# Kernel optimization log

Hardware: AMD Instinct MI355X
Metric: run time of the kernel (lower is better)

## Reference

```python
import jax, jax.numpy as jnp
import numpy as np

H = 16          # num_heads
TOP_K = 2
LN_EPS = 1e-5


def setup_inputs() -> dict:
    key = jax.random.key(0)
    ks = jax.random.split(key, 8)
    B, S, E, NE = 2, 1024, 1024, 8
    w = lambda k, shp: jax.random.normal(k, shp, dtype=jnp.float32) * 0.02
    return {
        "x": jax.random.normal(ks[0], (B, S, E), dtype=jnp.float32),
        "rW1": w(ks[1], (E // 2, E)),
        "rb1": jnp.zeros((E // 2,), jnp.float32),
        "ln_g": jnp.ones((E // 2,), jnp.float32),
        "ln_b": jnp.zeros((E // 2,), jnp.float32),
        "rW2": w(ks[2], (NE, E // 2)),
        "rb2": jnp.zeros((NE,), jnp.float32),
        "qW": w(ks[3], (NE, E, E)),
        "qb": jnp.zeros((NE, E), jnp.float32),
        "kW": w(ks[4], (NE, E, E)),
        "kb": jnp.zeros((NE, E), jnp.float32),
        "vW": w(ks[5], (NE, E, E)),
        "vb": jnp.zeros((NE, E), jnp.float32),
        "oW": w(ks[6], (NE, E, E)),
        "ob": jnp.zeros((NE, E), jnp.float32),
    }


def reference(x, rW1, rb1, ln_g, ln_b, rW2, rb2, qW, qb, kW, kb, vW, vb, oW, ob):
    B, S, E = x.shape
    NE = qW.shape[0]
    Dh = E // H
    scale = 1.0 / jnp.sqrt(jnp.asarray(Dh, x.dtype))

    # ---- router: Linear -> LayerNorm -> ReLU -> Linear ----
    h = x @ rW1.T + rb1                       # [B,S,E/2]
    mu = h.mean(-1, keepdims=True)
    var = ((h - mu) ** 2).mean(-1, keepdims=True)
    h = (h - mu) * jax.lax.rsqrt(var + LN_EPS) * ln_g + ln_b
    h = jax.nn.relu(h)
    logits = h @ rW2.T + rb2                  # [B,S,NE]
    probs = jax.nn.softmax(logits, axis=-1)

    # ---- top-k gating, renormalized, scattered to dense expert mask ----
    tp, ti = jax.lax.top_k(probs, TOP_K)      # [B,S,K]
    tp = tp / tp.sum(-1, keepdims=True)
    expert_mask = (jax.nn.one_hot(ti, NE, dtype=probs.dtype) * tp[..., None]).sum(-2)  # [B,S,NE]
    gates = jnp.moveaxis(expert_mask, -1, 0)  # [NE,B,S]

    # ---- every expert attends over all tokens; outputs gated and summed ----
    def expert_step(acc, params):
        qw, qb_, kw, kb_, vw, vb_, ow, ob_, g = params
        q = (x @ qw.T + qb_).reshape(B, S, H, Dh).transpose(0, 2, 1, 3)  # [B,H,S,Dh]
        k = (x @ kw.T + kb_).reshape(B, S, H, Dh).transpose(0, 2, 1, 3)
        v = (x @ vw.T + vb_).reshape(B, S, H, Dh).transpose(0, 2, 1, 3)
        scores = jnp.einsum("bhqd,bhkd->bhqk", q, k) * scale
        p = jax.nn.softmax(scores, axis=-1)
        o = jnp.einsum("bhqk,bhkd->bhqd", p, v)
        o = o.transpose(0, 2, 1, 3).reshape(B, S, E) @ ow.T + ob_
        return acc + o * g[..., None], None

    out, _ = jax.lax.scan(expert_step, jnp.zeros_like(x),
                          (qW, qb, kW, kb, vW, vb, oW, ob, gates))
    return out
```

## Files before the change

### kernel.cpp

```cpp
#include <hip/hip_runtime.h>
#include <hip/hip_bf16.h>

typedef unsigned short u16;
typedef unsigned int u32;
typedef __bf16 bf16x8 __attribute__((ext_vector_type(8)));
typedef float f32x4 __attribute__((ext_vector_type(4)));

__device__ __forceinline__ u16 f2bf(float f) {
  union { float f; unsigned u; } v; v.f = f;
  unsigned r = v.u + 0x7fffu + ((v.u >> 16) & 1u);
  return (u16)(r >> 16);
}

__device__ __forceinline__ f32x4 mfma16(bf16x8 a, bf16x8 b, f32x4 c) {
  return __builtin_amdgcn_mfma_f32_16x16x32_bf16(a, b, c, 0, 0, 0);
}

__device__ __forceinline__ void gl_lds16(const u16* g, u16* l) {
  __builtin_amdgcn_global_load_lds(
      (const __attribute__((address_space(1))) u32*)g,
      (__attribute__((address_space(3))) u32*)l, 16, 0, 0);
}

__global__ __launch_bounds__(256) void cvt_x_kernel(const float* __restrict__ x, u16* __restrict__ xb) {
  size_t i = (size_t)blockIdx.x * 256 + threadIdx.x;
  float4 v = reinterpret_cast<const float4*>(x)[i];
  unsigned long long pk = (unsigned long long)f2bf(v.x) |
                          ((unsigned long long)f2bf(v.y) << 16) |
                          ((unsigned long long)f2bf(v.z) << 32) |
                          ((unsigned long long)f2bf(v.w) << 48);
  *reinterpret_cast<unsigned long long*>(xb + i * 4) = pk;
}

__global__ __launch_bounds__(256) void cvt_w_kernel(
    const float* __restrict__ qW, const float* __restrict__ kW,
    const float* __restrict__ vW, const float* __restrict__ oW,
    u16* __restrict__ wb_qkv, u16* __restrict__ wb_o) {
  const size_t nqkv4 = (size_t)8 * 3 * 262144;
  const size_t total = nqkv4 + (size_t)8 * 262144;
  for (size_t i = (size_t)blockIdx.x * 256 + threadIdx.x; i < total;
       i += (size_t)gridDim.x * 256) {
    const float* src; u16* dst;
    if (i < nqkv4) {
      size_t elem = i * 4;
      size_t blk = elem >> 20;
      size_t el = blk / 3, ty = blk % 3;
      const float* W = (ty == 0 ? qW : (ty == 1 ? kW : vW));
      src = W + el * 1048576 + (elem & 1048575);
      dst = wb_qkv + elem;
    } else {
      size_t elem = (i - nqkv4) * 4;
      size_t el = elem >> 20;
      src = oW + el * 1048576 + (elem & 1048575);
      dst = wb_o + elem;
    }
    float4 v = *reinterpret_cast<const float4*>(src);
    unsigned long long pk = (unsigned long long)f2bf(v.x) |
                            ((unsigned long long)f2bf(v.y) << 16) |
                            ((unsigned long long)f2bf(v.z) << 32) |
                            ((unsigned long long)f2bf(v.w) << 48);
    *reinterpret_cast<unsigned long long*>(dst) = pk;
  }
}

__global__ __launch_bounds__(256) void zero_lists(u32* __restrict__ lists) {
  int i = blockIdx.x * 256 + threadIdx.x;
  if (i < 32784) lists[i] = 0;
}

__global__ __launch_bounds__(256) void router_gemm1(
    const float* __restrict__ x, const float* __restrict__ rW1,
    const float* __restrict__ rb1, float* __restrict__ hbuf) {
  __shared__ float aT[16][72];
  __shared__ float bT[16][72];
  int t = threadIdx.x;
  int tx = t & 15, ty = t >> 4;
  int m0 = blockIdx.x * 64, n0 = blockIdx.y * 64;
  float acc[4][4];
#pragma unroll
  for (int i = 0; i < 4; ++i)
#pragma unroll
    for (int j = 0; j < 4; ++j) acc[i][j] = 0.f;
  const float* Ab = x + (size_t)m0 * 1024;
  const float* Bb = rW1 + (size_t)n0 * 1024;
  int r = t >> 2, c4 = (t & 3) * 4;
  for (int k0 = 0; k0 < 1024; k0 += 16) {
    float4 av = *reinterpret_cast<const float4*>(Ab + (size_t)r * 1024 + k0 + c4);
    float4 bv = *reinterpret_cast<const float4*>(Bb + (size_t)r * 1024 + k0 + c4);
    aT[c4 + 0][r] = av.x; aT[c4 + 1][r] = av.y; aT[c4 + 2][r] = av.z; aT[c4 + 3][r] = av.w;
    bT[c4 + 0][r] = bv.x; bT[c4 + 1][r] = bv.y; bT[c4 + 2][r] = bv.z; bT[c4 + 3][r] = bv.w;
    __syncthreads();
#pragma unroll
    for (int kk = 0; kk < 16; ++kk) {
      float4 a = *reinterpret_cast<const float4*>(&aT[kk][ty * 4]);
      float4 b = *reinterpret_cast<const float4*>(&bT[kk][tx * 4]);
      float aa[4] = {a.x, a.y, a.z, a.w};
      float bb[4] = {b.x, b.y, b.z, b.w};
#pragma unroll
      for (int i = 0; i < 4; ++i)
#pragma unroll
        for (int j = 0; j < 4; ++j) acc[i][j] += aa[i] * bb[j];
    }
    __syncthreads();
  }
#pragma unroll
  for (int i = 0; i < 4; ++i) {
    int row = m0 + ty * 4 + i;
#pragma unroll
    for (int j = 0; j < 4; ++j) {
      int col = n0 + tx * 4 + j;
      hbuf[(size_t)row * 512 + col] = acc[i][j] + rb1[col];
    }
  }
}

__global__ __launch_bounds__(64) void router_finish(
    const float* __restrict__ hbuf, const float* __restrict__ ln_g,
    const float* __restrict__ ln_b, const float* __restrict__ rW2,
    const float* __restrict__ rb2,
    u32* __restrict__ tok_list, float* __restrict__ gate_list,
    u32* __restrict__ cnt, u32* __restrict__ inv) {
  int tok = blockIdx.x, lane = threadIdx.x;
  const float* hr = hbuf + (size_t)tok * 512;
  float4 v0 = *reinterpret_cast<const float4*>(hr + lane * 8);
  float4 v1 = *reinterpret_cast<const float4*>(hr + lane * 8 + 4);
  float hv[8] = {v0.x, v0.y, v0.z, v0.w, v1.x, v1.y, v1.z, v1.w};
  float s = 0.f;
#pragma unroll
  for (int j = 0; j < 8; ++j) s += hv[j];
#pragma unroll
  for (int m = 1; m < 64; m <<= 1) s += __shfl_xor(s, m);
  float mu = s * (1.0f / 512.0f);
  float s2 = 0.f;
#pragma unroll
  for (int j = 0; j < 8; ++j) { float d = hv[j] - mu; s2 += d * d; }
#pragma unroll
  for (int m = 1; m < 64; m <<= 1) s2 += __shfl_xor(s2, m);
  float rstd = 1.0f / sqrtf(s2 * (1.0f / 512.0f) + 1e-5f);
#pragma unroll
  for (int j = 0; j < 8; ++j) {
    float tv = (hv[j] - mu) * rstd * ln_g[lane * 8 + j] + ln_b[lane * 8 + j];
    hv[j] = fmaxf(tv, 0.0f);
  }
  float logit[8];
#pragma unroll
  for (int n = 0; n < 8; ++n) {
    const float* wr = rW2 + (size_t)n * 512 + lane * 8;
    float p = 0.f;
#pragma unroll
    for (int j = 0; j < 8; ++j) p += hv[j] * wr[j];
#pragma unroll
    for (int m = 1; m < 64; m <<= 1) p += __shfl_xor(p, m);
    logit[n] = p + rb2[n];
  }
  int i1 = 0; float l1 = logit[0];
#pragma unroll
  for (int n = 1; n < 8; ++n) if (logit[n] > l1) { l1 = logit[n]; i1 = n; }
  int i2 = -1; float l2 = -3.4e38f;
#pragma unroll
  for (int n = 0; n < 8; ++n) if (n != i1 && logit[n] > l2) { l2 = logit[n]; i2 = n; }
  float e2 = __expf(l2 - l1);
  float g1 = 1.0f / (1.0f + e2);
  float g2 = e2 * g1;
  if (lane == 0) {
    int b = tok >> 10, sq = tok & 1023;
    int p1 = i1 * 2 + b;
    u32 pos1 = atomicAdd(&cnt[p1], 1u);
    tok_list[p1 * 1024 + pos1] = (u32)sq;
    gate_list[p1 * 1024 + pos1] = g1;
    inv[tok * 2 + 0] = ((u32)p1 << 10) | pos1;
    int p2 = i2 * 2 + b;
    u32 pos2 = atomicAdd(&cnt[p2], 1u);
    tok_list[p2 * 1024 + pos2] = (u32)sq;
    gate_list[p2 * 1024 + pos2] = g2;
    inv[tok * 2 + 1] = ((u32)p2 << 10) | pos2;
  }
}

__device__ __forceinline__ void stage8(
    const u16* aS0, const u16* aS1, const u16* aS2, const u16* aS3,
    const u16* bS0, const u16* bS1, const u16* bS2, const u16* bS3,
    int k0, u16* aL, u16* bL, int w) {
  gl_lds16(aS0 + k0, aL + (32 * w + 0) * 64);
  gl_lds16(aS1 + k0, aL + (32 * w + 8) * 64);
  gl_lds16(aS2 + k0, aL + (32 * w + 16) * 64);
  gl_lds16(aS3 + k0, aL + (32 * w + 24) * 64);
  gl_lds16(bS0 + k0, bL + (32 * w + 0) * 64);
  gl_lds16(bS1 + k0, bL + (32 * w + 8) * 64);
  gl_lds16(bS2 + k0, bL + (32 * w + 16) * 64);
  gl_lds16(bS3 + k0, bL + (32 * w + 24) * 64);
}

__device__ __forceinline__ void gemm_mainloop_p(
    const u16* aS0, const u16* aS1, const u16* aS2, const u16* aS3,
    const u16* bS0, const u16* bS1, const u16* bS2, const u16* bS3,
    int K, u16* aL0, u16* bL0, u16* aL1, u16* bL1, f32x4 acc[4][4]) {
  const int t = threadIdx.x;
  const int w = t >> 6, lane = t & 63;
  const int wm = (w >> 1) * 64, wn = (w & 1) * 64;
  const int lr = lane & 15, lg = lane >> 4;
  const int T = K >> 6;
  stage8(aS0, aS1, aS2, aS3, bS0, bS1, bS2, bS3, 0, aL0, bL0, w);
  __syncthreads();
  for (int tt = 0; tt < T; ++tt) {
    u16* aC = (tt & 1) ? aL1 : aL0;
    u16* bC = (tt & 1) ? bL1 : bL0;
    if (tt + 1 < T) {
      u16* aN = (tt & 1) ? aL0 : aL1;
      u16* bN = (tt & 1) ? bL0 : bL1;
      stage8(aS0, aS1, aS2, aS3, bS0, bS1, bS2, bS3, (tt + 1) << 6, aN, bN, w);
    }
    __builtin_amdgcn_s_setprio(1);
#pragma unroll
    for (int kk = 0; kk < 2; ++kk) {
      bf16x8 af[4], bfr[4];
#pragma unroll
      for (int i = 0; i < 4; ++i) {
        int ra = wm + i * 16 + lr;
        af[i] = *reinterpret_cast<const bf16x8*>(aC + ra * 64 + (((kk * 4 + lg) ^ (ra & 7)) << 3));
        int rb = wn + i * 16 + lr;
        bfr[i] = *reinterpret_cast<const bf16x8*>(bC + rb * 64 + (((kk * 4 + lg) ^ (rb & 7)) << 3));
      }
#pragma unroll
      for (int mi = 0; mi < 4; ++mi)
#pragma unroll
        for (int ni = 0; ni < 4; ++ni)
          acc[mi][ni] = mfma16(af[mi], bfr[ni], acc[mi][ni]);
    }
    __builtin_amdgcn_s_setprio(0);
    __syncthreads();
  }
}

__global__ __launch_bounds__(256) void kv_gemm_kernel(
    const u16* __restrict__ xb, const u16* __restrict__ wb_qkv,
    const float* __restrict__ kb, const float* __restrict__ vb,
    u16* __restrict__ kbuf, u16* __restrict__ vtbuf) {
  __shared__ u16 lds[32768];
  int orig = blockIdx.x;
  int wgid = (orig & 7) * 256 + (orig >> 3);
  int e = wgid >> 8, r = wgid & 255;
  int ty = r >> 7, rr = r & 127;
  const int t = threadIdx.x, w = t >> 6, lane = t & 63;
  const int rloc = lane >> 3, cloc = lane & 7;
  const int sc8 = (cloc ^ rloc) * 8;
  const u16 *A, *B;
  int mblk, nblk;
  if (ty == 0) {
    mblk = rr >> 3; nblk = rr & 7;
    A = xb + (size_t)mblk * 128 * 1024;
    B = wb_qkv + (size_t)(e * 3 + 1) * 1048576 + (size_t)nblk * 128 * 1024;
  } else {
    mblk = rr & 7; nblk = rr >> 3;
    A = wb_qkv + (size_t)(e * 3 + 2) * 1048576 + (size_t)mblk * 128 * 1024;
    B = xb + (size_t)nblk * 128 * 1024;
  }
  f32x4 acc[4][4];
#pragma unroll
  for (int i = 0; i < 4; ++i)
#pragma unroll
    for (int j = 0; j < 4; ++j) { f32x4 z = {0.f, 0.f, 0.f, 0.f}; acc[i][j] = z; }
  gemm_mainloop_p(
      A + (size_t)(32 * w + 0 + rloc) * 1024 + sc8, A + (size_t)(32 * w + 8 + rloc) * 1024 + sc8,
      A + (size_t)(32 * w + 16 + rloc) * 1024 + sc8, A + (size_t)(32 * w + 24 + rloc) * 1024 + sc8,
      B + (size_t)(32 * w + 0 + rloc) * 1024 + sc8, B + (size_t)(32 * w + 8 + rloc) * 1024 + sc8,
      B + (size_t)(32 * w + 16 + rloc) * 1024 + sc8, B + (size_t)(32 * w + 24 + rloc) * 1024 + sc8,
      1024, lds, lds + 8192, lds + 16384, lds + 24576, acc);
  const int wm = (w >> 1) * 64, wn = (w & 1) * 64;
  const int lr = lane & 15, lg = lane >> 4;
  if (ty == 0) {
    const float* bias = kb + (size_t)e * 1024 + nblk * 128;
    u16* Cb = kbuf + ((size_t)e * 2048 + (size_t)mblk * 128) * 1024 + nblk * 128;
#pragma unroll
    for (int ni = 0; ni < 4; ++ni) {
      int lcol = wn + ni * 16 + lr;
      float bv = bias[lcol];
#pragma unroll
      for (int mi = 0; mi < 4; ++mi)
#pragma unroll
        for (int rg = 0; rg < 4; ++rg) {
          int lrow = wm + mi * 16 + lg * 4 + rg;
          Cb[(size_t)lrow * 1024 + lcol] = f2bf(acc[mi][ni][rg] + bv);
        }
    }
  } else {
    const float* bias = vb + (size_t)e * 1024 + mblk * 128;
    int bb = nblk >> 3, nn = nblk & 7;
    u16* Cb = vtbuf + ((size_t)(e * 2 + bb) * 1024 + (size_t)mblk * 128) * 1024 + nn * 128;
#pragma unroll
    for (int ni = 0; ni < 4; ++ni) {
      int lcol = wn + ni * 16 + lr;
#pragma unroll
      for (int mi = 0; mi < 4; ++mi)
#pragma unroll
        for (int rg = 0; rg < 4; ++rg) {
          int lrow = wm + mi * 16 + lg * 4 + rg;
          Cb[(size_t)lrow * 1024 + lcol] = f2bf(acc[mi][ni][rg] + bias[lrow]);
        }
    }
  }
}

__global__ __launch_bounds__(256) void q_gemm_kernel(
    const u16* __restrict__ xb, const u16* __restrict__ wb_qkv,
    const float* __restrict__ qb, const u32* __restrict__ tok_list,
    const u32* __restrict__ cnt, u16* __restrict__ qc) {
  __shared__ u16 lds[32768];
  int nblk = blockIdx.x, mt = blockIdx.y, p = blockIdx.z;
  int c = (int)cnt[p];
  if (mt * 128 >= c) return;
  int e = p >> 1, b = p & 1;
  const int t = threadIdx.x, w = t >> 6, lane = t & 63;
  const int rloc = lane >> 3, cloc = lane & 7;
  const int sc8 = (cloc ^ rloc) * 8;
  const u32* tl = tok_list + p * 1024 + mt * 128 + 32 * w + rloc;
  int t0 = (int)(tl[0] & 1023), t1 = (int)(tl[8] & 1023);
  int t2 = (int)(tl[16] & 1023), t3 = (int)(tl[24] & 1023);
  const u16* Ab = xb + (size_t)b * 1024 * 1024 + sc8;
  const u16* B = wb_qkv + (size_t)(e * 3) * 1048576 + (size_t)nblk * 128 * 1024;
  f32x4 acc[4][4];
#pragma unroll
  for (int i = 0; i < 4; ++i)
#pragma unroll
    for (int j = 0; j < 4; ++j) { f32x4 z = {0.f, 0.f, 0.f, 0.f}; acc[i][j] = z; }
  gemm_mainloop_p(
      Ab + (size_t)t0 * 1024, Ab + (size_t)t1 * 1024, Ab + (size_t)t2 * 1024, Ab + (size_t)t3 * 1024,
      B + (size_t)(32 * w + 0 + rloc) * 1024 + sc8, B + (size_t)(32 * w + 8 + rloc) * 1024 + sc8,
      B + (size_t)(32 * w + 16 + rloc) * 1024 + sc8, B + (size_t)(32 * w + 24 + rloc) * 1024 + sc8,
      1024, lds, lds + 8192, lds + 16384, lds + 24576, acc);
  const int wm = (w >> 1) * 64, wn = (w & 1) * 64;
  const int lr = lane & 15, lg = lane >> 4;
  const float* bias = qb + (size_t)e * 1024 + nblk * 128;
  u16* Cb = qc + ((size_t)p * 1024 + (size_t)mt * 128) * 1024 + nblk * 128;
#pragma unroll
  for (int ni = 0; ni < 4; ++ni) {
    int lcol = wn + ni * 16 + lr;
    float bv = bias[lcol];
#pragma unroll
    for (int mi = 0; mi < 4; ++mi)
#pragma unroll
      for (int rg = 0; rg < 4; ++rg) {
        int lrow = wm + mi * 16 + lg * 4 + rg;
        Cb[(size_t)lrow * 1024 + lcol] = f2bf(acc[mi][ni][rg] + bv);
      }
  }
}

__global__ __launch_bounds__(256) void attn_kernel(
    const u16* __restrict__ qc, const u16* __restrict__ kbuf,
    const u16* __restrict__ vtbuf, const u32* __restrict__ cnt,
    u16* __restrict__ oc) {
  __shared__ u16 Kl[2][4096];
  __shared__ u16 Vtl[2][4096];
  __shared__ u16 Pl[4096];
  int h = blockIdx.x;
  int p = blockIdx.y >> 3, lt = blockIdx.y & 7;
  int c = (int)cnt[p];
  if (lt * 64 >= c) return;
  int e = p >> 1, b = p & 1;
  const u16* Qb = qc + ((size_t)p * 1024 + (size_t)lt * 64) * 1024 + h * 64;
  const u16* Kg = kbuf + ((size_t)e * 2048 + (size_t)b * 1024) * 1024 + h * 64;
  const u16* Vtg = vtbuf + ((size_t)(e * 2 + b) * 1024 + (size_t)h * 64) * 1024;
  u16* Og = oc + ((size_t)p * 1024 + (size_t)lt * 64) * 1024 + h * 64;
  const int t = threadIdx.x, w = t >> 6, lane = t & 63;
  const int lr = lane & 15, lg = lane >> 4;
  const int rloc = lane >> 3, kc = lane & 7;

#define STAGE_ATTN(IT, KB, VB)                                                   \
  {                                                                              \
    int kv0_ = (IT) * 64;                                                        \
    _Pragma("unroll")                                                            \
    for (int r_ = 0; r_ < 2; ++r_) {                                             \
      int row_ = 16 * w + 8 * r_ + rloc;                                         \
      gl_lds16(Kg + (size_t)(kv0_ + row_) * 1024 + (kc ^ (row_ & 7)) * 8,        \
               (KB) + (16 * w + 8 * r_) * 64);                                   \
      gl_lds16(Vtg + (size_t)row_ * 1024 + kv0_ + (kc ^ (row_ & 7)) * 8,         \
               (VB) + (16 * w + 8 * r_) * 64);                                   \
    }                                                                            \
  }

  STAGE_ATTN(0, Kl[0], Vtl[0]);

  bf16x8 qa0 = *reinterpret_cast<const bf16x8*>(Qb + (size_t)(w * 16 + lr) * 1024 + lg * 8);
  bf16x8 qa1 = *reinterpret_cast<const bf16x8*>(Qb + (size_t)(w * 16 + lr) * 1024 + 32 + lg * 8);

  f32x4 oacc[4];
  float mrun[4], lsum[4];
#pragma unroll
  for (int i = 0; i < 4; ++i) {
    f32x4 z = {0.f, 0.f, 0.f, 0.f}; oacc[i] = z; mrun[i] = -3.4e38f; lsum[i] = 0.f;
  }
  __syncthreads();

  for (int it = 0; it < 16; ++it) {
    const int cur = it & 1;
    const u16* Kc = Kl[cur];
    const u16* Vc = Vtl[cur];
    if (it + 1 < 16) STAGE_ATTN(it + 1, Kl[cur ^ 1], Vtl[cur ^ 1]);
    f32x4 sv[4];
    __builtin_amdgcn_s_setprio(1);
#pragma unroll
    for (int nt = 0; nt < 4; ++nt) {
      f32x4 z = {0.f, 0.f, 0.f, 0.f};
#pragma unroll
      for (int kk = 0; kk < 2; ++kk) {
        int rk = nt * 16 + lr;
        bf16x8 kf = *reinterpret_cast<const bf16x8*>(Kc + rk * 64 + (((kk * 4 + lg) ^ (rk & 7)) << 3));
        z = mfma16(kk ? qa1 : qa0, kf, z);
      }
      sv[nt] = z * 0.125f;
    }
    __builtin_amdgcn_s_setprio(0);
#pragma unroll
    for (int rg = 0; rg < 4; ++rg) {
      float tm = fmaxf(fmaxf(sv[0][rg], sv[1][rg]), fmaxf(sv[2][rg], sv[3][rg]));
#pragma unroll
      for (int mm = 1; mm < 16; mm <<= 1) tm = fmaxf(tm, __shfl_xor(tm, mm));
      float mn = fmaxf(mrun[rg], tm);
      float al = __expf(mrun[rg] - mn);
      mrun[rg] = mn;
      lsum[rg] *= al;
#pragma unroll
      for (int nt = 0; nt < 4; ++nt) oacc[nt][rg] *= al;
    }
#pragma unroll
    for (int nt = 0; nt < 4; ++nt) {
#pragma unroll
      for (int rg = 0; rg < 4; ++rg) {
        float pv = __expf(sv[nt][rg] - mrun[rg]);
        lsum[rg] += pv;
        int prow = lg * 4 + rg;
        Pl[w * 1024 + prow * 64 + ((nt * 16 + lr) ^ ((prow & 7) << 3))] = f2bf(pv);
      }
    }
    __builtin_amdgcn_s_setprio(1);
#pragma unroll
    for (int kk = 0; kk < 2; ++kk) {
      bf16x8 pf = *reinterpret_cast<const bf16x8*>(
          Pl + w * 1024 + lr * 64 + (((kk * 4 + lg) ^ (lr & 7)) << 3));
#pragma unroll
      for (int nt = 0; nt < 4; ++nt) {
        int rv = nt * 16 + lr;
        bf16x8 vf = *reinterpret_cast<const bf16x8*>(Vc + rv * 64 + (((kk * 4 + lg) ^ (rv & 7)) << 3));
        oacc[nt] = mfma16(pf, vf, oacc[nt]);
      }
    }
    __builtin_amdgcn_s_setprio(0);
    __syncthreads();
  }
#pragma unroll
  for (int rg = 0; rg < 4; ++rg) {
#pragma unroll
    for (int mm = 1; mm < 16; mm <<= 1) lsum[rg] += __shfl_xor(lsum[rg], mm);
    float inv = 1.0f / lsum[rg];
#pragma unroll
    for (int nt = 0; nt < 4; ++nt)
      Og[(size_t)(w * 16 + lg * 4 + rg) * 1024 + nt * 16 + lr] = f2bf(oacc[nt][rg] * inv);
  }
#undef STAGE_ATTN
}

__global__ __launch_bounds__(256) void oproj_kernel(
    const u16* __restrict__ oc, const u16* __restrict__ wb_o,
    const u32* __restrict__ cnt, float* __restrict__ projc) {
  __shared__ u16 lds[32768];
  int nblk = blockIdx.x, mt = blockIdx.y, p = blockIdx.z;
  int c = (int)cnt[p];
  if (mt * 128 >= c) return;
  int e = p >> 1;
  const int t = threadIdx.x, w = t >> 6, lane = t & 63;
  const int rloc = lane >> 3, cloc = lane & 7;
  const int sc8 = (cloc ^ rloc) * 8;
  const u16* A = oc + ((size_t)p * 1024 + (size_t)mt * 128) * 1024;
  const u16* B = wb_o + (size_t)e * 1048576 + (size_t)nblk * 128 * 1024;
  f32x4 acc[4][4];
#pragma unroll
  for (int i = 0; i < 4; ++i)
#pragma unroll
    for (int j = 0; j < 4; ++j) { f32x4 z = {0.f, 0.f, 0.f, 0.f}; acc[i][j] = z; }
  gemm_mainloop_p(
      A + (size_t)(32 * w + 0 + rloc) * 1024 + sc8, A + (size_t)(32 * w + 8 + rloc) * 1024 + sc8,
      A + (size_t)(32 * w + 16 + rloc) * 1024 + sc8, A + (size_t)(32 * w + 24 + rloc) * 1024 + sc8,
      B + (size_t)(32 * w + 0 + rloc) * 1024 + sc8, B + (size_t)(32 * w + 8 + rloc) * 1024 + sc8,
      B + (size_t)(32 * w + 16 + rloc) * 1024 + sc8, B + (size_t)(32 * w + 24 + rloc) * 1024 + sc8,
      1024, lds, lds + 8192, lds + 16384, lds + 24576, acc);
  const int wm = (w >> 1) * 64, wn = (w & 1) * 64;
  const int lr = lane & 15, lg = lane >> 4;
  float* Pb = projc + ((size_t)p * 1024 + (size_t)mt * 128) * 1024 + nblk * 128;
#pragma unroll
  for (int mi = 0; mi < 4; ++mi)
#pragma unroll
    for (int rg = 0; rg < 4; ++rg) {
      int lrow = wm + mi * 16 + lg * 4 + rg;
#pragma unroll
      for (int ni = 0; ni < 4; ++ni) {
        int lcol = wn + ni * 16 + lr;
        Pb[(size_t)lrow * 1024 + lcol] = acc[mi][ni][rg];
      }
    }
}

__global__ __launch_bounds__(256) void merge_out(
    const float* __restrict__ projc, const float* __restrict__ ob,
    const float* __restrict__ gate_list, const u32* __restrict__ inv,
    float* __restrict__ out) {
  int tok = blockIdx.x;
  int c4 = threadIdx.x * 4;
  u32 i1 = inv[tok * 2], i2 = inv[tok * 2 + 1];
  int idx1 = (int)(i1 >> 10) * 1024 + (int)(i1 & 1023);
  int idx2 = (int)(i2 >> 10) * 1024 + (int)(i2 & 1023);
  float g1 = gate_list[idx1], g2 = gate_list[idx2];
  int e1 = (int)(i1 >> 11), e2 = (int)(i2 >> 11);
  float4 a = *reinterpret_cast<const float4*>(projc + (size_t)idx1 * 1024 + c4);
  float4 bvec = *reinterpret_cast<const float4*>(projc + (size_t)idx2 * 1024 + c4);
  float4 o1 = *reinterpret_cast<const float4*>(ob + (size_t)e1 * 1024 + c4);
  float4 o2 = *reinterpret_cast<const float4*>(ob + (size_t)e2 * 1024 + c4);
  float4 r;
  r.x = g1 * (a.x + o1.x) + g2 * (bvec.x + o2.x);
  r.y = g1 * (a.y + o1.y) + g2 * (bvec.y + o2.y);
  r.z = g1 * (a.z + o1.z) + g2 * (bvec.z + o2.z);
  r.w = g1 * (a.w + o1.w) + g2 * (bvec.w + o2.w);
  *reinterpret_cast<float4*>(out + (size_t)tok * 1024 + c4) = r;
}

extern "C" void kernel_launch(void* const* d_in, const int* in_sizes, int n_in,
                              void* d_out, int out_size, void* d_ws, size_t ws_size,
                              hipStream_t stream) {
  const float* x    = (const float*)d_in[0];
  const float* rW1  = (const float*)d_in[1];
  const float* rb1  = (const float*)d_in[2];
  const float* ln_g = (const float*)d_in[3];
  const float* ln_b = (const float*)d_in[4];
  const float* rW2  = (const float*)d_in[5];
  const float* rb2  = (const float*)d_in[6];
  const float* qW   = (const float*)d_in[7];
  const float* qb   = (const float*)d_in[8];
  const float* kW   = (const float*)d_in[9];
  const float* kb   = (const float*)d_in[10];
  const float* vW   = (const float*)d_in[11];
  const float* vb   = (const float*)d_in[12];
  const float* oW   = (const float*)d_in[13];
  const float* ob   = (const float*)d_in[14];
  float* out = (float*)d_out;

  const size_t need = 50331648ull + 16777216ull + 67108864ull + 33554432ull +
                      33554432ull + 4194304ull + 147520ull;
  if (ws_size < need) return;
  char* pp = (char*)d_ws;
  u16* wb_qkv = (u16*)pp; pp += 50331648ull;
  u16* wb_o   = (u16*)pp; pp += 16777216ull;
  u16* kbuf   = (u16*)pp; pp += 33554432ull;
  u16* vtbuf  = (u16*)pp; pp += 33554432ull;
  u16* qc     = (u16*)pp; pp += 33554432ull;
  u16* oc     = (u16*)pp; pp += 33554432ull;
  u16* xb     = (u16*)pp; pp += 4194304ull;
  u32* lists  = (u32*)pp;
  u32* tok_list    = lists;
  float* gate_list = (float*)(lists + 16384);
  u32* cnt         = lists + 32768;
  u32* inv         = lists + 32784;
  float* hbuf  = (float*)qc;
  float* projc = (float*)kbuf;

  cvt_x_kernel<<<dim3(2048), dim3(256), 0, stream>>>(x, xb);
  cvt_w_kernel<<<dim3(2048), dim3(256), 0, stream>>>(qW, kW, vW, oW, wb_qkv, wb_o);
  router_gemm1<<<dim3(32, 8), dim3(256), 0, stream>>>(x, rW1, rb1, hbuf);
  zero_lists<<<dim3(129), dim3(256), 0, stream>>>(lists);
  router_finish<<<dim3(2048), dim3(64), 0, stream>>>(hbuf, ln_g, ln_b, rW2, rb2,
                                                     tok_list, gate_list, cnt, inv);
  kv_gemm_kernel<<<dim3(2048), dim3(256), 0, stream>>>(xb, wb_qkv, kb, vb, kbuf, vtbuf);
  q_gemm_kernel<<<dim3(8, 8, 16), dim3(256), 0, stream>>>(xb, wb_qkv, qb, tok_list, cnt, qc);
  attn_kernel<<<dim3(16, 128), dim3(256), 0, stream>>>(qc, kbuf, vtbuf, cnt, oc);
  oproj_kernel<<<dim3(8, 8, 16), dim3(256), 0, stream>>>(oc, wb_o, cnt, projc);
  merge_out<<<dim3(2048), dim3(256), 0, stream>>>(projc, ob, gate_list, inv, out);
}
```

Before: 485.3 us.

## Use 64-row M tiles for routed Q and O GEMMs, fuse list zeroing

Adds a 64x128-tile GEMM mainloop and switches the routed Q-projection and O-projection kernels to it. This halves per-block M granularity, which cuts padded work on each expert's ragged token count and roughly doubles grid occupancy. It also folds list zeroing into the x-conversion kernel to drop one launch, and doubles the K step in the router GEMM1 to halve barriers. Smaller tiles lower per-block arithmetic intensity, so weight tiles are reloaded more often.

```diff
diff --git a/kernel.cpp b/kernel.cpp
--- a/kernel.cpp
+++ b/kernel.cpp
@@ -22,8 +22,11 @@
       (__attribute__((address_space(3))) u32*)l, 16, 0, 0);
 }
 
-__global__ __launch_bounds__(256) void cvt_x_kernel(const float* __restrict__ x, u16* __restrict__ xb) {
+__global__ __launch_bounds__(256) void cvt_x_kernel(const float* __restrict__ x,
+                                                    u16* __restrict__ xb,
+                                                    u32* __restrict__ lists) {
   size_t i = (size_t)blockIdx.x * 256 + threadIdx.x;
+  if (i < 32784) lists[i] = 0;
   float4 v = reinterpret_cast<const float4*>(x)[i];
   unsigned long long pk = (unsigned long long)f2bf(v.x) |
                           ((unsigned long long)f2bf(v.y) << 16) |
@@ -63,16 +66,11 @@
   }
 }
 
-__global__ __launch_bounds__(256) void zero_lists(u32* __restrict__ lists) {
-  int i = blockIdx.x * 256 + threadIdx.x;
-  if (i < 32784) lists[i] = 0;
-}
-
 __global__ __launch_bounds__(256) void router_gemm1(
     const float* __restrict__ x, const float* __restrict__ rW1,
     const float* __restrict__ rb1, float* __restrict__ hbuf) {
-  __shared__ float aT[16][72];
-  __shared__ float bT[16][72];
+  __shared__ float aT[32][72];
+  __shared__ float bT[32][72];
   int t = threadIdx.x;
   int tx = t & 15, ty = t >> 4;
   int m0 = blockIdx.x * 64, n0 = blockIdx.y * 64;
@@ -83,15 +81,19 @@
     for (int j = 0; j < 4; ++j) acc[i][j] = 0.f;
   const float* Ab = x + (size_t)m0 * 1024;
   const float* Bb = rW1 + (size_t)n0 * 1024;
-  int r = t >> 2, c4 = (t & 3) * 4;
-  for (int k0 = 0; k0 < 1024; k0 += 16) {
-    float4 av = *reinterpret_cast<const float4*>(Ab + (size_t)r * 1024 + k0 + c4);
-    float4 bv = *reinterpret_cast<const float4*>(Bb + (size_t)r * 1024 + k0 + c4);
-    aT[c4 + 0][r] = av.x; aT[c4 + 1][r] = av.y; aT[c4 + 2][r] = av.z; aT[c4 + 3][r] = av.w;
-    bT[c4 + 0][r] = bv.x; bT[c4 + 1][r] = bv.y; bT[c4 + 2][r] = bv.z; bT[c4 + 3][r] = bv.w;
+  int r = t >> 2, c8 = (t & 3) * 8;
+  for (int k0 = 0; k0 < 1024; k0 += 32) {
+    float4 av0 = *reinterpret_cast<const float4*>(Ab + (size_t)r * 1024 + k0 + c8);
+    float4 av1 = *reinterpret_cast<const float4*>(Ab + (size_t)r * 1024 + k0 + c8 + 4);
+    float4 bv0 = *reinterpret_cast<const float4*>(Bb + (size_t)r * 1024 + k0 + c8);
+    float4 bv1 = *reinterpret_cast<const float4*>(Bb + (size_t)r * 1024 + k0 + c8 + 4);
+    aT[c8 + 0][r] = av0.x; aT[c8 + 1][r] = av0.y; aT[c8 + 2][r] = av0.z; aT[c8 + 3][r] = av0.w;
+    aT[c8 + 4][r] = av1.x; aT[c8 + 5][r] = av1.y; aT[c8 + 6][r] = av1.z; aT[c8 + 7][r] = av1.w;
+    bT[c8 + 0][r] = bv0.x; bT[c8 + 1][r] = bv0.y; bT[c8 + 2][r] = bv0.z; bT[c8 + 3][r] = bv0.w;
+    bT[c8 + 4][r] = bv1.x; bT[c8 + 5][r] = bv1.y; bT[c8 + 6][r] = bv1.z; bT[c8 + 7][r] = bv1.w;
     __syncthreads();
 #pragma unroll
-    for (int kk = 0; kk < 16; ++kk) {
+    for (int kk = 0; kk < 32; ++kk) {
       float4 a = *reinterpret_cast<const float4*>(&aT[kk][ty * 4]);
       float4 b = *reinterpret_cast<const float4*>(&bT[kk][tx * 4]);
       float aa[4] = {a.x, a.y, a.z, a.w};
@@ -225,6 +227,61 @@
       for (int mi = 0; mi < 4; ++mi)
 #pragma unroll
         for (int ni = 0; ni < 4; ++ni)
+          acc[mi][ni] = mfma16(af[mi], bfr[ni], acc[mi][ni]);
+    }
+    __builtin_amdgcn_s_setprio(0);
+    __syncthreads();
+  }
+}
+
+__device__ __forceinline__ void stage6(
+    const u16* aS0, const u16* aS1,
+    const u16* bS0, const u16* bS1, const u16* bS2, const u16* bS3,
+    int k0, u16* aL, u16* bL, int w) {
+  gl_lds16(aS0 + k0, aL + (16 * w + 0) * 64);
+  gl_lds16(aS1 + k0, aL + (16 * w + 8) * 64);
+  gl_lds16(bS0 + k0, bL + (32 * w + 0) * 64);
+  gl_lds16(bS1 + k0, bL + (32 * w + 8) * 64);
+  gl_lds16(bS2 + k0, bL + (32 * w + 16) * 64);
+  gl_lds16(bS3 + k0, bL + (32 * w + 24) * 64);
+}
+
+__device__ __forceinline__ void gemm_mainloop64(
+    const u16* aS0, const u16* aS1,
+    const u16* bS0, const u16* bS1, const u16* bS2, const u16* bS3,
+    int K, u16* aL0, u16* bL0, u16* aL1, u16* bL1, f32x4 acc[4][2]) {
+  const int t = threadIdx.x;
+  const int w = t >> 6, lane = t & 63;
+  const int lr = lane & 15, lg = lane >> 4;
+  const int T = K >> 6;
+  stage6(aS0, aS1, bS0, bS1, bS2, bS3, 0, aL0, bL0, w);
+  __syncthreads();
+  for (int tt = 0; tt < T; ++tt) {
+    u16* aC = (tt & 1) ? aL1 : aL0;
+    u16* bC = (tt & 1) ? bL1 : bL0;
+    if (tt + 1 < T) {
+      u16* aN = (tt & 1) ? aL0 : aL1;
+      u16* bN = (tt & 1) ? bL0 : bL1;
+      stage6(aS0, aS1, bS0, bS1, bS2, bS3, (tt + 1) << 6, aN, bN, w);
+    }
+    __builtin_amdgcn_s_setprio(1);
+#pragma unroll
+    for (int kk = 0; kk < 2; ++kk) {
+      bf16x8 af[4], bfr[2];
+#pragma unroll
+      for (int i = 0; i < 4; ++i) {
+        int ra = i * 16 + lr;
+        af[i] = *reinterpret_cast<const bf16x8*>(aC + ra * 64 + (((kk * 4 + lg) ^ (ra & 7)) << 3));
+      }
+#pragma unroll
+      for (int j = 0; j < 2; ++j) {
+        int rb = w * 32 + j * 16 + lr;
+        bfr[j] = *reinterpret_cast<const bf16x8*>(bC + rb * 64 + (((kk * 4 + lg) ^ (rb & 7)) << 3));
+      }
+#pragma unroll
+      for (int mi = 0; mi < 4; ++mi)
+#pragma unroll
+        for (int ni = 0; ni < 2; ++ni)
           acc[mi][ni] = mfma16(af[mi], bfr[ni], acc[mi][ni]);
     }
     __builtin_amdgcn_s_setprio(0);
@@ -305,42 +362,40 @@
     const u16* __restrict__ xb, const u16* __restrict__ wb_qkv,
     const float* __restrict__ qb, const u32* __restrict__ tok_list,
     const u32* __restrict__ cnt, u16* __restrict__ qc) {
-  __shared__ u16 lds[32768];
+  __shared__ u16 lds[24576];
   int nblk = blockIdx.x, mt = blockIdx.y, p = blockIdx.z;
   int c = (int)cnt[p];
-  if (mt * 128 >= c) return;
+  if (mt * 64 >= c) return;
   int e = p >> 1, b = p & 1;
   const int t = threadIdx.x, w = t >> 6, lane = t & 63;
   const int rloc = lane >> 3, cloc = lane & 7;
   const int sc8 = (cloc ^ rloc) * 8;
-  const u32* tl = tok_list + p * 1024 + mt * 128 + 32 * w + rloc;
+  const u32* tl = tok_list + p * 1024 + mt * 64 + 16 * w + rloc;
   int t0 = (int)(tl[0] & 1023), t1 = (int)(tl[8] & 1023);
-  int t2 = (int)(tl[16] & 1023), t3 = (int)(tl[24] & 1023);
   const u16* Ab = xb + (size_t)b * 1024 * 1024 + sc8;
   const u16* B = wb_qkv + (size_t)(e * 3) * 1048576 + (size_t)nblk * 128 * 1024;
-  f32x4 acc[4][4];
+  f32x4 acc[4][2];
 #pragma unroll
   for (int i = 0; i < 4; ++i)
 #pragma unroll
-    for (int j = 0; j < 4; ++j) { f32x4 z = {0.f, 0.f, 0.f, 0.f}; acc[i][j] = z; }
-  gemm_mainloop_p(
-      Ab + (size_t)t0 * 1024, Ab + (size_t)t1 * 1024, Ab + (size_t)t2 * 1024, Ab + (size_t)t3 * 1024,
+    for (int j = 0; j < 2; ++j) { f32x4 z = {0.f, 0.f, 0.f, 0.f}; acc[i][j] = z; }
+  gemm_mainloop64(
+      Ab + (size_t)t0 * 1024, Ab + (size_t)t1 * 1024,
       B + (size_t)(32 * w + 0 + rloc) * 1024 + sc8, B + (size_t)(32 * w + 8 + rloc) * 1024 + sc8,
       B + (size_t)(32 * w + 16 + rloc) * 1024 + sc8, B + (size_t)(32 * w + 24 + rloc) * 1024 + sc8,
-      1024, lds, lds + 8192, lds + 16384, lds + 24576, acc);
-  const int wm = (w >> 1) * 64, wn = (w & 1) * 64;
+      1024, lds, lds + 8192, lds + 4096, lds + 16384, acc);
   const int lr = lane & 15, lg = lane >> 4;
   const float* bias = qb + (size_t)e * 1024 + nblk * 128;
-  u16* Cb = qc + ((size_t)p * 1024 + (size_t)mt * 128) * 1024 + nblk * 128;
-#pragma unroll
-  for (int ni = 0; ni < 4; ++ni) {
-    int lcol = wn + ni * 16 + lr;
+  u16* Cb = qc + ((size_t)p * 1024 + (size_t)mt * 64) * 1024 + nblk * 128;
+#pragma unroll
+  for (int ni = 0; ni < 2; ++ni) {
+    int lcol = w * 32 + ni * 16 + lr;
     float bv = bias[lcol];
 #pragma unroll
     for (int mi = 0; mi < 4; ++mi)
 #pragma unroll
       for (int rg = 0; rg < 4; ++rg) {
-        int lrow = wm + mi * 16 + lg * 4 + rg;
+        int lrow = mi * 16 + lg * 4 + rg;
         Cb[(size_t)lrow * 1024 + lcol] = f2bf(acc[mi][ni][rg] + bv);
       }
   }
@@ -463,38 +518,36 @@
 __global__ __launch_bounds__(256) void oproj_kernel(
     const u16* __restrict__ oc, const u16* __restrict__ wb_o,
     const u32* __restrict__ cnt, float* __restrict__ projc) {
-  __shared__ u16 lds[32768];
+  __shared__ u16 lds[24576];
   int nblk = blockIdx.x, mt = blockIdx.y, p = blockIdx.z;
   int c = (int)cnt[p];
-  if (mt * 128 >= c) return;
+  if (mt * 64 >= c) return;
   int e = p >> 1;
   const int t = threadIdx.x, w = t >> 6, lane = t & 63;
   const int rloc = lane >> 3, cloc = lane & 7;
   const int sc8 = (cloc ^ rloc) * 8;
-  const u16* A = oc + ((size_t)p * 1024 + (size_t)mt * 128) * 1024;
+  const u16* A = oc + ((size_t)p * 1024 + (size_t)mt * 64) * 1024;
   const u16* B = wb_o + (size_t)e * 1048576 + (size_t)nblk * 128 * 1024;
-  f32x4 acc[4][4];
+  f32x4 acc[4][2];
 #pragma unroll
   for (int i = 0; i < 4; ++i)
 #pragma unroll
-    for (int j = 0; j < 4; ++j) { f32x4 z = {0.f, 0.f, 0.f, 0.f}; acc[i][j] = z; }
-  gemm_mainloop_p(
-      A + (size_t)(32 * w + 0 + rloc) * 1024 + sc8, A + (size_t)(32 * w + 8 + rloc) * 1024 + sc8,
-      A + (size_t)(32 * w + 16 + rloc) * 1024 + sc8, A + (size_t)(32 * w + 24 + rloc) * 1024 + sc8,
+    for (int j = 0; j < 2; ++j) { f32x4 z = {0.f, 0.f, 0.f, 0.f}; acc[i][j] = z; }
+  gemm_mainloop64(
+      A + (size_t)(16 * w + 0 + rloc) * 1024 + sc8, A + (size_t)(16 * w + 8 + rloc) * 1024 + sc8,
       B + (size_t)(32 * w + 0 + rloc) * 1024 + sc8, B + (size_t)(32 * w + 8 + rloc) * 1024 + sc8,
       B + (size_t)(32 * w + 16 + rloc) * 1024 + sc8, B + (size_t)(32 * w + 24 + rloc) * 1024 + sc8,
-      1024, lds, lds + 8192, lds + 16384, lds + 24576, acc);
-  const int wm = (w >> 1) * 64, wn = (w & 1) * 64;
+      1024, lds, lds + 8192, lds + 4096, lds + 16384, acc);
   const int lr = lane & 15, lg = lane >> 4;
-  float* Pb = projc + ((size_t)p * 1024 + (size_t)mt * 128) * 1024 + nblk * 128;
+  float* Pb = projc + ((size_t)p * 1024 + (size_t)mt * 64) * 1024 + nblk * 128;
 #pragma unroll
   for (int mi = 0; mi < 4; ++mi)
 #pragma unroll
     for (int rg = 0; rg < 4; ++rg) {
-      int lrow = wm + mi * 16 + lg * 4 + rg;
-#pragma unroll
-      for (int ni = 0; ni < 4; ++ni) {
-        int lcol = wn + ni * 16 + lr;
+      int lrow = mi * 16 + lg * 4 + rg;
+#pragma unroll
+      for (int ni = 0; ni < 2; ++ni) {
+        int lcol = w * 32 + ni * 16 + lr;
         Pb[(size_t)lrow * 1024 + lcol] = acc[mi][ni][rg];
       }
     }
@@ -562,15 +615,14 @@
   float* hbuf  = (float*)qc;
   float* projc = (float*)kbuf;
 
-  cvt_x_kernel<<<dim3(2048), dim3(256), 0, stream>>>(x, xb);
+  cvt_x_kernel<<<dim3(2048), dim3(256), 0, stream>>>(x, xb, lists);
   cvt_w_kernel<<<dim3(2048), dim3(256), 0, stream>>>(qW, kW, vW, oW, wb_qkv, wb_o);
   router_gemm1<<<dim3(32, 8), dim3(256), 0, stream>>>(x, rW1, rb1, hbuf);
-  zero_lists<<<dim3(129), dim3(256), 0, stream>>>(lists);
   router_finish<<<dim3(2048), dim3(64), 0, stream>>>(hbuf, ln_g, ln_b, rW2, rb2,
                                                      tok_list, gate_list, cnt, inv);
   kv_gemm_kernel<<<dim3(2048), dim3(256), 0, stream>>>(xb, wb_qkv, kb, vb, kbuf, vtbuf);
-  q_gemm_kernel<<<dim3(8, 8, 16), dim3(256), 0, stream>>>(xb, wb_qkv, qb, tok_list, cnt, qc);
+  q_gemm_kernel<<<dim3(8, 16, 16), dim3(256), 0, stream>>>(xb, wb_qkv, qb, tok_list, cnt, qc);
   attn_kernel<<<dim3(16, 128), dim3(256), 0, stream>>>(qc, kbuf, vtbuf, cnt, oc);
-  oproj_kernel<<<dim3(8, 8, 16), dim3(256), 0, stream>>>(oc, wb_o, cnt, projc);
+  oproj_kernel<<<dim3(8, 16, 16), dim3(256), 0, stream>>>(oc, wb_o, cnt, projc);
   merge_out<<<dim3(2048), dim3(256), 0, stream>>>(projc, ob, gate_list, inv, out);
 }
```

Result: no change. 480.8 us (-0.9%).
